# Kernel tuning notes

Measured on AMD Instinct MI355X. Metric: run time of the kernel, lower is better.

## Reference

```python
import jax, jax.numpy as jnp
import numpy as np

B, T, S, D, H, E, K, FF = 4, 1024, 1024, 1024, 16, 8, 2, 4096
DH = D // H
EPS = 1e-5

def layernorm(x, g, b):
    m = x.mean(-1, keepdims=True)
    v = x.var(-1, keepdims=True)
    return (x - m) / jnp.sqrt(v + EPS) * g + b

def mha(q, k, v, mask, wq, bq, wk, bk, wv, bv, wo, bo):
    Bq, Tq, _ = q.shape
    Tk = k.shape[1]
    Q = (q @ wq + bq).reshape(Bq, Tq, H, DH).transpose(0, 2, 1, 3)
    Kh = (k @ wk + bk).reshape(Bq, Tk, H, DH).transpose(0, 2, 1, 3)
    V = (v @ wv + bv).reshape(Bq, Tk, H, DH).transpose(0, 2, 1, 3)
    scores = jnp.einsum('bhqd,bhkd->bhqk', Q, Kh) / (DH ** 0.5)
    scores = jnp.where(mask != 0, scores, jnp.float32(-1e9))
    A = jax.nn.softmax(scores, axis=-1)
    O = jnp.einsum('bhqk,bhkd->bhqd', A, V).transpose(0, 2, 1, 3).reshape(Bq, Tq, D)
    return O @ wo + bo

def sparse_moe(x, wg, bg, w1, b1, w2, b2):
    # x: [B,T,D] -> tokens [N,D]
    Bx, Tx, _ = x.shape
    xt = x.reshape(-1, D)
    N = xt.shape[0]
    probs = jax.nn.softmax(xt @ wg + bg, axis=-1)          # [N,E]
    topv, topi = jax.lax.top_k(probs, K)                    # [N,K]
    topv = topv / topv.sum(-1, keepdims=True)
    gates = jnp.zeros((N, E), xt.dtype).at[jnp.arange(N)[:, None], topi].set(topv)
    h = jax.nn.relu(jnp.einsum('nd,edh->enh', xt, w1) + b1[:, None, :])  # [E,N,FF]
    y = jnp.einsum('enh,ehd->end', h, w2) + b2[:, None, :]               # [E,N,D]
    out = jnp.einsum('ne,end->nd', gates, y)
    return out.reshape(Bx, Tx, D)

def setup_inputs() -> dict:
    key = jax.random.key(0)
    ks = jax.random.split(key, 32)
    r = lambda k, s: jax.random.normal(k, s, dtype=jnp.float32) * 0.02
    inp = {
        'x': jax.random.normal(ks[0], (B, T, D), jnp.float32),
        'encoder_out': jax.random.normal(ks[1], (B, S, D), jnp.float32),
        'src_attn_mask': jnp.ones((B, 1, 1, S), jnp.int32),
        'tgt_attn_mask': jnp.tril(jnp.ones((T, T), jnp.int32))[None, None],
        'ln1_g': jnp.ones((D,), jnp.float32), 'ln1_b': jnp.zeros((D,), jnp.float32),
        'ln2_g': jnp.ones((D,), jnp.float32), 'ln2_b': jnp.zeros((D,), jnp.float32),
        'ln3_g': jnp.ones((D,), jnp.float32), 'ln3_b': jnp.zeros((D,), jnp.float32),
        'wq1': r(ks[2], (D, D)), 'bq1': jnp.zeros((D,), jnp.float32),
        'wk1': r(ks[3], (D, D)), 'bk1': jnp.zeros((D,), jnp.float32),
        'wv1': r(ks[4], (D, D)), 'bv1': jnp.zeros((D,), jnp.float32),
        'wo1': r(ks[5], (D, D)), 'bo1': jnp.zeros((D,), jnp.float32),
        'wq2': r(ks[6], (D, D)), 'bq2': jnp.zeros((D,), jnp.float32),
        'wk2': r(ks[7], (D, D)), 'bk2': jnp.zeros((D,), jnp.float32),
        'wv2': r(ks[8], (D, D)), 'bv2': jnp.zeros((D,), jnp.float32),
        'wo2': r(ks[9], (D, D)), 'bo2': jnp.zeros((D,), jnp.float32),
        'wg': r(ks[10], (D, E)), 'bg': jnp.zeros((E,), jnp.float32),
        'w1': r(ks[11], (E, D, FF)), 'b1': jnp.zeros((E, FF), jnp.float32),
        'w2': r(ks[12], (E, FF, D)), 'b2': jnp.zeros((E, D), jnp.float32),
    }
    return inp

def reference(x, encoder_out, src_attn_mask, tgt_attn_mask,
              ln1_g, ln1_b, ln2_g, ln2_b, ln3_g, ln3_b,
              wq1, bq1, wk1, bk1, wv1, bv1, wo1, bo1,
              wq2, bq2, wk2, bk2, wv2, bv2, wo2, bo2,
              wg, bg, w1, b1, w2, b2):
    # pre-norm residual: x + sublayer(LN(x)); dropout=0 (eval)
    n1 = layernorm(x, ln1_g, ln1_b)
    h1 = x + mha(n1, n1, n1, tgt_attn_mask, wq1, bq1, wk1, bk1, wv1, bv1, wo1, bo1)
    n2 = layernorm(h1, ln2_g, ln2_b)
    h2 = h1 + mha(n2, encoder_out, encoder_out, src_attn_mask, wq2, bq2, wk2, bk2, wv2, bv2, wo2, bo2)
    n3 = layernorm(h2, ln3_g, ln3_b)
    h3 = h2 + sparse_moe(n3, wg, bg, w1, b1, w2, b2)
    return h3
```

## Files before the change

kernel.cpp:

```cpp
#include <hip/hip_runtime.h>

typedef unsigned short u16;
typedef float f32x4 __attribute__((ext_vector_type(4)));
typedef short s16x8 __attribute__((ext_vector_type(8)));
typedef u16   u16x4 __attribute__((ext_vector_type(4)));

#define DEV static __device__ __forceinline__

DEV u16 f2b(float f){
  unsigned u = __builtin_bit_cast(unsigned, f);
  u += 0x7fffu + ((u >> 16) & 1u);
  return (u16)(u >> 16);
}
DEV float b2f(u16 h){ unsigned u = ((unsigned)h) << 16; return __builtin_bit_cast(float, u); }
DEV void tsplit(float v, u16& hv, u16& lv){
  unsigned u = __builtin_bit_cast(unsigned, v);
  hv = (u16)(u >> 16);
  float rest = v - __builtin_bit_cast(float, u & 0xffff0000u);
  lv = (u16)(__builtin_bit_cast(unsigned, rest) >> 16);
}
DEV float fexp2(float x){ float r; asm("v_exp_f32 %0, %1" : "=v"(r) : "v"(x)); return r; }

DEV void glds16(const u16* g, u16* l){
  __builtin_amdgcn_global_load_lds(
      (const __attribute__((address_space(1))) void*)g,
      (__attribute__((address_space(3))) void*)l, 16, 0, 0);
}

DEV f32x4 mfma3(s16x8 ah, s16x8 al, s16x8 bh, s16x8 bl, f32x4 c){
  c = __builtin_amdgcn_mfma_f32_16x16x32_bf16(ah, bh, c, 0, 0, 0);
  c = __builtin_amdgcn_mfma_f32_16x16x32_bf16(ah, bl, c, 0, 0, 0);
  c = __builtin_amdgcn_mfma_f32_16x16x32_bf16(al, bh, c, 0, 0, 0);
  return c;
}

constexpr int TT = 1024, DM = 1024, NE = 8, FFD = 4096;
constexpr int NTOK = 4096;

struct Ptr8 { const float* p[8]; };

__global__ __launch_bounds__(256) void trans8_k(Ptr8 srcs, u16* __restrict__ dh, u16* __restrict__ dl){
  __shared__ float tl[64][65];
  const float* src = srcs.p[blockIdx.z];
  u16* dsth = dh + (size_t)blockIdx.z * 1024 * 1024;
  u16* dstl = dl + (size_t)blockIdx.z * 1024 * 1024;
  const int tid = threadIdx.x;
  const int r0 = blockIdx.y * 64, c0 = blockIdx.x * 64;
  const int ty = tid >> 4, tx = tid & 15;
#pragma unroll
  for (int i = 0; i < 4; i++){
    int row = ty + i * 16;
    f32x4 v = *(const f32x4*)&src[(size_t)(r0 + row) * 1024 + c0 + tx * 4];
#pragma unroll
    for (int j = 0; j < 4; j++) tl[row][tx * 4 + j] = v[j];
  }
  __syncthreads();
#pragma unroll
  for (int i = 0; i < 4; i++){
    int drow = ty + i * 16;
    u16x4 oh, ol;
#pragma unroll
    for (int j = 0; j < 4; j++){
      float v = tl[tx * 4 + j][drow];
      u16 hh, ll; tsplit(v, hh, ll);
      oh[j] = hh; ol[j] = ll;
    }
    *(u16x4*)&dsth[(size_t)(c0 + drow) * 1024 + r0 + tx * 4] = oh;
    *(u16x4*)&dstl[(size_t)(c0 + drow) * 1024 + r0 + tx * 4] = ol;
  }
}

__global__ __launch_bounds__(256) void transb_k(const float* __restrict__ src0, u16* __restrict__ dst0, int R, int C){
  __shared__ float tl[64][65];
  const float* src = src0 + (size_t)blockIdx.z * R * C;
  u16* dst = dst0 + (size_t)blockIdx.z * R * C;
  const int tid = threadIdx.x;
  const int r0 = blockIdx.y * 64, c0 = blockIdx.x * 64;
  const int ty = tid >> 4, tx = tid & 15;
#pragma unroll
  for (int i = 0; i < 4; i++){
    int row = ty + i * 16;
    f32x4 v = *(const f32x4*)&src[(size_t)(r0 + row) * C + c0 + tx * 4];
#pragma unroll
    for (int j = 0; j < 4; j++) tl[row][tx * 4 + j] = v[j];
  }
  __syncthreads();
#pragma unroll
  for (int i = 0; i < 4; i++){
    int drow = ty + i * 16;
    u16x4 o;
#pragma unroll
    for (int j = 0; j < 4; j++) o[j] = f2b(tl[tx * 4 + j][drow]);
    *(u16x4*)&dst[(size_t)(c0 + drow) * R + r0 + tx * 4] = o;
  }
}

__global__ __launch_bounds__(256) void split_k(const float* __restrict__ src,
                                               u16* __restrict__ dh, u16* __restrict__ dl, int n4){
  int i = blockIdx.x * 256 + threadIdx.x;
  if (i < n4){
    f32x4 v = *(const f32x4*)&src[(size_t)i * 4];
    u16x4 oh, ol;
#pragma unroll
    for (int j = 0; j < 4; j++){ u16 hh, ll; tsplit(v[j], hh, ll); oh[j] = hh; ol[j] = ll; }
    *(u16x4*)&dh[(size_t)i * 4] = oh;
    *(u16x4*)&dl[(size_t)i * 4] = ol;
  }
}

__global__ __launch_bounds__(256) void ln_k(const float* __restrict__ x, const float* __restrict__ g,
                                            const float* __restrict__ b,
                                            u16* __restrict__ outH, u16* __restrict__ outL){
  __shared__ float red[8];
  const int row = blockIdx.x, tid = threadIdx.x, l = tid & 63, wave = tid >> 6;
  f32x4 v = *(const f32x4*)&x[(size_t)row * DM + tid * 4];
  float s = v[0] + v[1] + v[2] + v[3];
  float sq = v[0]*v[0] + v[1]*v[1] + v[2]*v[2] + v[3]*v[3];
#pragma unroll
  for (int m = 1; m < 64; m <<= 1){ s += __shfl_xor(s, m); sq += __shfl_xor(sq, m); }
  if (l == 0){ red[wave] = s; red[4 + wave] = sq; }
  __syncthreads();
  float tot = red[0] + red[1] + red[2] + red[3];
  float totq = red[4] + red[5] + red[6] + red[7];
  float mean = tot * (1.0f / DM);
  float var = totq * (1.0f / DM) - mean * mean;
  float rstd = rsqrtf(var + 1e-5f);
  f32x4 gg = *(const f32x4*)&g[tid * 4];
  f32x4 bb = *(const f32x4*)&b[tid * 4];
  u16x4 oh, ol;
#pragma unroll
  for (int j = 0; j < 4; j++){
    float y = (v[j] - mean) * rstd * gg[j] + bb[j];
    u16 hh, ll; tsplit(y, hh, ll); oh[j] = hh; ol[j] = ll;
  }
  *(u16x4*)&outH[(size_t)row * DM + tid * 4] = oh;
  if (outL) *(u16x4*)&outL[(size_t)row * DM + tid * 4] = ol;
}

struct QKVArgs {
  const u16* ah[3]; const u16* al[3]; const float* bias[3];
};

__global__ __launch_bounds__(512) void gemm_qkv3_k(
    QKVArgs args, const u16* __restrict__ Bhp, const u16* __restrict__ Blp,
    u16* __restrict__ QH, u16* __restrict__ QL,
    u16* __restrict__ KH, u16* __restrict__ KL,
    u16* __restrict__ VTH, u16* __restrict__ VTL)
{
  constexpr int K = DM;
  __shared__ alignas(16) u16 LAh[2][128 * 32], LAl[2][128 * 32];
  __shared__ alignas(16) u16 LBh[2][128 * 32], LBl[2][128 * 32];
  const int tid = threadIdx.x, l = tid & 63, wave = tid >> 6;
  const int id = blockIdx.x;
  const int mlo = id & 7, nb = (id >> 3) & 7, mhi = (id >> 6) & 3, seg = id >> 8;
  const int m0 = (mlo + 8 * mhi) * 128, n0 = nb * 128;
  const int r0 = tid >> 2, seg8 = (tid & 3) * 8;
  const u16* gAh = args.ah[seg] + (size_t)(m0 + r0) * K + seg8;
  const u16* gAl = args.al[seg] + (size_t)(m0 + r0) * K + seg8;
  const u16* gBh = Bhp + (size_t)(seg * 1024 + n0 + r0) * K + seg8;
  const u16* gBl = Blp + (size_t)(seg * 1024 + n0 + r0) * K + seg8;
  u16* wAh0 = &LAh[0][wave * 512]; u16* wAh1 = &LAh[1][wave * 512];
  u16* wAl0 = &LAl[0][wave * 512]; u16* wAl1 = &LAl[1][wave * 512];
  u16* wBh0 = &LBh[0][wave * 512]; u16* wBh1 = &LBh[1][wave * 512];
  u16* wBl0 = &LBl[0][wave * 512]; u16* wBl1 = &LBl[1][wave * 512];
  f32x4 acc[4][2];
#pragma unroll
  for (int i = 0; i < 4; i++)
#pragma unroll
    for (int j = 0; j < 2; j++) acc[i][j] = f32x4{0.f, 0.f, 0.f, 0.f};
  const int wm = (wave >> 2) * 64, wn = (wave & 3) * 32;
  for (int kt = 0; kt < K; kt += 64){
    __syncthreads();
    glds16(gAh + kt, wAh0); glds16(gAh + kt + 32, wAh1);
    glds16(gAl + kt, wAl0); glds16(gAl + kt + 32, wAl1);
    glds16(gBh + kt, wBh0); glds16(gBh + kt + 32, wBh1);
    glds16(gBl + kt, wBl0); glds16(gBl + kt + 32, wBl1);
    __syncthreads();
#pragma unroll
    for (int p = 0; p < 2; p++){
      s16x8 afh[4], afl[4], bfh[2], bfl[2];
#pragma unroll
      for (int i = 0; i < 4; i++){
        int ar = (wm + i * 16 + (l & 15)) * 32 + (l >> 4) * 8;
        afh[i] = *(const s16x8*)&LAh[p][ar];
        afl[i] = *(const s16x8*)&LAl[p][ar];
      }
#pragma unroll
      for (int j = 0; j < 2; j++){
        int br = (wn + j * 16 + (l & 15)) * 32 + (l >> 4) * 8;
        bfh[j] = *(const s16x8*)&LBh[p][br];
        bfl[j] = *(const s16x8*)&LBl[p][br];
      }
#pragma unroll
      for (int i = 0; i < 4; i++)
#pragma unroll
        for (int j = 0; j < 2; j++)
          acc[i][j] = mfma3(afh[i], afl[i], bfh[j], bfl[j], acc[i][j]);
    }
  }
  const float* bp = args.bias[seg];
  u16* DH = (seg == 0) ? QH : KH;
  u16* DL = (seg == 0) ? QL : KL;
#pragma unroll
  for (int i = 0; i < 4; i++)
#pragma unroll
    for (int r = 0; r < 4; r++){
      int row = m0 + wm + i * 16 + (l >> 4) * 4 + r;
#pragma unroll
      for (int j = 0; j < 2; j++){
        int col = n0 + wn + j * 16 + (l & 15);
        float v = acc[i][j][r] + bp[col];
        u16 hv, lv; tsplit(v, hv, lv);
        if (seg == 2){
          int bb = row >> 10, tq = row & 1023, hh = col >> 6, dd = col & 63;
          size_t vi = ((size_t)((bb << 4) + hh) * 64 + dd) * 1024 + tq;
          VTH[vi] = hv; VTL[vi] = lv;
        } else {
          size_t idx = (size_t)row * 1024 + col;
          DH[idx] = hv; DL[idx] = lv;
        }
      }
    }
}

__global__ __launch_bounds__(256) void gemm_o64_k(
    const u16* __restrict__ Ahp, const u16* __restrict__ Alp,
    const u16* __restrict__ Bhp, const u16* __restrict__ Blp,
    const float* __restrict__ bias, const float* __restrict__ res,
    float* __restrict__ Cf)
{
  constexpr int K = DM;
  __shared__ alignas(16) u16 LAh[64 * 32], LAl[64 * 32];
  __shared__ alignas(16) u16 LBh[64 * 32], LBl[64 * 32];
  const int tid = threadIdx.x, l = tid & 63, wave = tid >> 6;
  const int m0 = blockIdx.y * 64, n0 = blockIdx.x * 64;
  const int rA = tid >> 2, seg8 = (tid & 3) * 8;
  const u16* gAh = Ahp + (size_t)(m0 + rA) * K + seg8;
  const u16* gAl = Alp + (size_t)(m0 + rA) * K + seg8;
  const u16* gBh = Bhp + (size_t)(n0 + rA) * K + seg8;
  const u16* gBl = Blp + (size_t)(n0 + rA) * K + seg8;
  u16* wAh = &LAh[wave * 512]; u16* wAl = &LAl[wave * 512];
  u16* wBh = &LBh[wave * 512]; u16* wBl = &LBl[wave * 512];
  f32x4 acc[2][2];
#pragma unroll
  for (int i = 0; i < 2; i++)
#pragma unroll
    for (int j = 0; j < 2; j++) acc[i][j] = f32x4{0.f, 0.f, 0.f, 0.f};
  const int wm = (wave >> 1) * 32, wn = (wave & 1) * 32;
  for (int kt = 0; kt < K; kt += 32){
    __syncthreads();
    glds16(gAh + kt, wAh);
    glds16(gAl + kt, wAl);
    glds16(gBh + kt, wBh);
    glds16(gBl + kt, wBl);
    __syncthreads();
    s16x8 afh[2], afl[2], bfh[2], bfl[2];
#pragma unroll
    for (int i = 0; i < 2; i++){
      int ar = (wm + i * 16 + (l & 15)) * 32 + (l >> 4) * 8;
      afh[i] = *(const s16x8*)&LAh[ar];
      afl[i] = *(const s16x8*)&LAl[ar];
    }
#pragma unroll
    for (int j = 0; j < 2; j++){
      int br = (wn + j * 16 + (l & 15)) * 32 + (l >> 4) * 8;
      bfh[j] = *(const s16x8*)&LBh[br];
      bfl[j] = *(const s16x8*)&LBl[br];
    }
#pragma unroll
    for (int i = 0; i < 2; i++)
#pragma unroll
      for (int j = 0; j < 2; j++)
        acc[i][j] = mfma3(afh[i], afl[i], bfh[j], bfl[j], acc[i][j]);
  }
#pragma unroll
  for (int i = 0; i < 2; i++)
#pragma unroll
    for (int r = 0; r < 4; r++){
      int row = m0 + wm + i * 16 + (l >> 4) * 4 + r;
#pragma unroll
      for (int j = 0; j < 2; j++){
        int col = n0 + wn + j * 16 + (l & 15);
        size_t idx = (size_t)row * 1024 + col;
        Cf[idx] = acc[i][j][r] + bias[col] + res[idx];
      }
    }
}

template<bool CAUSAL>
__global__ __launch_bounds__(512) void attn5_k(
    const u16* __restrict__ Qh, const u16* __restrict__ Ql,
    const u16* __restrict__ Kh, const u16* __restrict__ Kl,
    const u16* __restrict__ Vth, const u16* __restrict__ Vtl,
    const int* __restrict__ mask,
    float* __restrict__ OP0, float* __restrict__ OP1,
    float* __restrict__ LS0, float* __restrict__ LS1,
    int Tq, int Tk)
{
  constexpr float CS = 0.125f * 1.4426950408889634f;
  __shared__ alignas(16) u16 KhiL[2048], KloL[2048];
  __shared__ alignas(16) u16 VhiL[2048], VloL[2048];
  __shared__ alignas(16) u16 Plh[8][640], Pll[8][640];
  const int tid = threadIdx.x, l = tid & 63, wave = tid >> 6;
  const int id = blockIdx.x;
  const int bh = ((id >> 3) & 7) * 8 + (id & 7);
  const int b = bh >> 4, h = bh & 15;
  const int qt = (id >> 6) & 7, ks = id >> 9;
  const int q0 = qt * 128;
  float* __restrict__ OP = ks ? OP1 : OP0;
  float* __restrict__ LS = ks ? LS1 : LS0;
  const int ktBeg = ks * 512;
  int lim = CAUSAL ? (q0 + 128) : Tk;
  if (lim > Tk) lim = Tk;
  int ktEnd = (ks + 1) * 512;
  if (ktEnd > lim) ktEnd = lim;

  const int qr = q0 + wave * 16 + (l & 15);
  s16x8 qah[2], qal[2];
#pragma unroll
  for (int kb = 0; kb < 2; kb++){
    size_t base = (size_t)(b * Tq + qr) * DM + h * 64 + kb * 32 + (l >> 4) * 8;
    qah[kb] = *(const s16x8*)(Qh + base);
    qal[kb] = *(const s16x8*)(Ql + base);
  }

  const int sHalf = wave >> 2;
  const int sw = wave & 3;
  const int iS = sw * 64 + l;
  const int keyS = iS >> 3, cKS = iS & 7;
  const u16* gK = (sHalf ? Kl : Kh)
      + (size_t)(b * Tk + ktBeg + keyS) * DM + h * 64 + ((cKS ^ (keyS & 7)) * 8);
  u16* dK = (sHalf ? KloL : KhiL) + sw * 512;
  const int dS = iS >> 2, cVS = iS & 3;
  const size_t vgbase = (size_t)bh * 64 * 1024;
  const u16* gV = (sHalf ? Vtl : Vth)
      + vgbase + (size_t)dS * 1024 + ktBeg + ((cVS ^ ((dS >> 1) & 3)) * 8);
  u16* dV = (sHalf ? VloL : VhiL) + sw * 512;

  float lsum[4] = {0.f, 0.f, 0.f, 0.f};
  f32x4 oacc[4];
#pragma unroll
  for (int nb = 0; nb < 4; nb++) oacc[nb] = f32x4{0.f, 0.f, 0.f, 0.f};
  const int qgr = q0 + wave * 16 + (l >> 4) * 4;

  for (int kt = ktBeg; kt < ktEnd; kt += 32){
    __syncthreads();
    glds16(gK, dK); gK += (size_t)32 * DM;
    glds16(gV, dV); gV += 32;
    __syncthreads();

    f32x4 s[2];
#pragma unroll
    for (int n = 0; n < 2; n++){
      s[n] = f32x4{0.f, 0.f, 0.f, 0.f};
      const int key = n * 16 + (l & 15);
      const int sK = (key & 7);
#pragma unroll
      for (int kb = 0; kb < 2; kb++){
        const int cK = kb * 4 + (l >> 4);
        const int off = key * 64 + ((cK ^ sK) * 8);
        s16x8 kh = *(const s16x8*)&KhiL[off];
        s16x8 klo = *(const s16x8*)&KloL[off];
        s[n] = __builtin_amdgcn_mfma_f32_16x16x32_bf16(qah[kb], kh, s[n], 0, 0, 0);
        s[n] = __builtin_amdgcn_mfma_f32_16x16x32_bf16(qah[kb], klo, s[n], 0, 0, 0);
        s[n] = __builtin_amdgcn_mfma_f32_16x16x32_bf16(qal[kb], kh, s[n], 0, 0, 0);
      }
    }
    int key0 = kt + (l & 15), key1 = key0 + 16;
    int mv0 = 1, mv1 = 1;
    if (!CAUSAL && mask){ mv0 = mask[b * Tk + key0]; mv1 = mask[b * Tk + key1]; }
#pragma unroll
    for (int r = 0; r < 4; r++){
      float p0, p1;
      if (CAUSAL){
        int qg = qgr + r;
        p0 = (key0 <= qg) ? fexp2(s[0][r] * CS) : 0.f;
        p1 = (key1 <= qg) ? fexp2(s[1][r] * CS) : 0.f;
      } else {
        p0 = mv0 ? fexp2(s[0][r] * CS) : 0.f;
        p1 = mv1 ? fexp2(s[1][r] * CS) : 0.f;
      }
      lsum[r] += p0 + p1;
      int po = ((l >> 4) * 4 + r) * 40 + (l & 15);
      u16 h0, l0, h1, l1;
      tsplit(p0, h0, l0); tsplit(p1, h1, l1);
      Plh[wave][po] = h0;      Pll[wave][po] = l0;
      Plh[wave][po + 16] = h1; Pll[wave][po + 16] = l1;
    }
    s16x8 pah = *(const s16x8*)&Plh[wave][(l & 15) * 40 + (l >> 4) * 8];
    s16x8 pal = *(const s16x8*)&Pll[wave][(l & 15) * 40 + (l >> 4) * 8];
#pragma unroll
    for (int nb = 0; nb < 4; nb++){
      const int d = nb * 16 + (l & 15);
      const int off = d * 32 + (((l >> 4) ^ ((d >> 1) & 3)) * 8);
      s16x8 vfh = *(const s16x8*)&VhiL[off];
      s16x8 vfl = *(const s16x8*)&VloL[off];
      oacc[nb] = mfma3(pah, pal, vfh, vfl, oacc[nb]);
    }
  }
#pragma unroll
  for (int r = 0; r < 4; r++){
    float s = lsum[r];
    s += __shfl_xor(s, 1); s += __shfl_xor(s, 2);
    s += __shfl_xor(s, 4); s += __shfl_xor(s, 8);
    int qg = qgr + r;
    if ((l & 15) == 0) LS[(size_t)bh * 1024 + qg] = s;
#pragma unroll
    for (int nb = 0; nb < 4; nb++)
      OP[(size_t)(b * Tq + qg) * DM + h * 64 + nb * 16 + (l & 15)] = oacc[nb][r];
  }
}

__global__ __launch_bounds__(256) void norm_k(
    const float* __restrict__ OP0, const float* __restrict__ OP1,
    const float* __restrict__ LS0, const float* __restrict__ LS1,
    u16* __restrict__ Oh, u16* __restrict__ Ol)
{
  const int t = blockIdx.x, c = threadIdx.x * 4;
  const int b = t >> 10, q = t & 1023, h = c >> 6;
  const size_t li = (size_t)(b * 16 + h) * 1024 + q;
  float inv = 1.0f / (LS0[li] + LS1[li]);
  f32x4 o0 = *(const f32x4*)&OP0[(size_t)t * DM + c];
  f32x4 o1 = *(const f32x4*)&OP1[(size_t)t * DM + c];
  u16x4 oh, ol;
#pragma unroll
  for (int j = 0; j < 4; j++){
    float v = (o0[j] + o1[j]) * inv;
    u16 hh, ll; tsplit(v, hh, ll); oh[j] = hh; ol[j] = ll;
  }
  *(u16x4*)&Oh[(size_t)t * DM + c] = oh;
  *(u16x4*)&Ol[(size_t)t * DM + c] = ol;
}

__global__ __launch_bounds__(256) void moe_gate_k(const float* __restrict__ X,
    const float* __restrict__ g3, const float* __restrict__ b3,
    const float* __restrict__ wg, const float* __restrict__ bg,
    int* __restrict__ cnt, int* __restrict__ perm,
    int* __restrict__ toke, int* __restrict__ tokp, float* __restrict__ tokg)
{
  const int wave = threadIdx.x >> 6, l = threadIdx.x & 63;
  const int t = blockIdx.x * 4 + wave;
  float xv[16];
  float s = 0.f, sq = 0.f;
#pragma unroll
  for (int i = 0; i < 16; i++){
    xv[i] = X[(size_t)t * DM + l + i * 64];
    s += xv[i]; sq += xv[i] * xv[i];
  }
#pragma unroll
  for (int m = 1; m < 64; m <<= 1){ s += __shfl_xor(s, m); sq += __shfl_xor(sq, m); }
  float mean = s * (1.0f / DM);
  float var = sq * (1.0f / DM) - mean * mean;
  float rstd = rsqrtf(var + 1e-5f);
  float acc[8];
#pragma unroll
  for (int e = 0; e < 8; e++) acc[e] = 0.f;
#pragma unroll
  for (int i = 0; i < 16; i++){
    int k = l + i * 64;
    float xn = (xv[i] - mean) * rstd * g3[k] + b3[k];
    f32x4 wa = *(const f32x4*)&wg[k * 8];
    f32x4 wb = *(const f32x4*)&wg[k * 8 + 4];
#pragma unroll
    for (int j = 0; j < 4; j++){ acc[j] += xn * wa[j]; acc[4 + j] += xn * wb[j]; }
  }
#pragma unroll
  for (int e = 0; e < 8; e++)
#pragma unroll
    for (int m = 1; m < 64; m <<= 1) acc[e] += __shfl_xor(acc[e], m);
  if (l == 0){
    float lg[8];
#pragma unroll
    for (int e = 0; e < 8; e++) lg[e] = acc[e] + bg[e];
    float mx = lg[0];
#pragma unroll
    for (int e = 1; e < 8; e++) mx = fmaxf(mx, lg[e]);
    float ex[8]; float sum = 0.f;
#pragma unroll
    for (int e = 0; e < 8; e++){ ex[e] = expf(lg[e] - mx); sum += ex[e]; }
    int i0 = 0;
    for (int e = 1; e < 8; e++) if (ex[e] > ex[i0]) i0 = e;
    int i1 = (i0 == 0) ? 1 : 0;
    for (int e = 0; e < 8; e++) if (e != i0 && ex[e] > ex[i1]) i1 = e;
    float p0 = ex[i0] / sum, p1 = ex[i1] / sum;
    float gs = p0 + p1;
    int pos0 = atomicAdd(&cnt[i0], 1);
    int pos1 = atomicAdd(&cnt[i1], 1);
    perm[i0 * 4096 + pos0] = t;
    perm[i1 * 4096 + pos1] = t;
    toke[2 * t] = i0; toke[2 * t + 1] = i1;
    tokp[2 * t] = pos0; tokp[2 * t + 1] = pos1;
    tokg[2 * t] = p0 / gs; tokg[2 * t + 1] = p1 / gs;
  }
}

__global__ void offsets_k(const int* __restrict__ cnt, int* __restrict__ off){
  if (threadIdx.x == 0){
    int a = 0;
    for (int e = 0; e < 8; e++){ off[e] = a; a += cnt[e]; }
  }
}

__global__ __launch_bounds__(512) void gemm_moe1_k(
    const u16* __restrict__ X, const u16* __restrict__ W1t, const float* __restrict__ b1,
    const int* __restrict__ perm, const int* __restrict__ cnt, const int* __restrict__ off,
    u16* __restrict__ Hb)
{
  const int id = blockIdx.x;
  const int e = id & 7;
  const int rest = id >> 3;
  const int n0 = (rest & 31) * 128;
  const int mt = rest >> 5;
  const int Ce = cnt[e];
  if (mt * 128 >= Ce) return;
  __shared__ alignas(16) u16 Asl[2][128 * 32];
  __shared__ alignas(16) u16 Bsl[2][128 * 32];
  const int tid = threadIdx.x, l = tid & 63, wave = tid >> 6;
  const int r0 = tid >> 2, seg = (tid & 3) * 8;
  const int rl = mt * 128 + r0;
  const int g = perm[e * 4096 + (rl < Ce ? rl : Ce - 1)];
  const u16* gA = X + (size_t)g * DM + seg;
  const u16* gB = W1t + (size_t)e * FFD * DM + (size_t)(n0 + r0) * DM + seg;
  u16* wA0 = &Asl[0][wave * 512]; u16* wA1 = &Asl[1][wave * 512];
  u16* wB0 = &Bsl[0][wave * 512]; u16* wB1 = &Bsl[1][wave * 512];
  f32x4 acc[4][2];
#pragma unroll
  for (int i = 0; i < 4; i++)
#pragma unroll
    for (int j = 0; j < 2; j++) acc[i][j] = f32x4{0.f,0.f,0.f,0.f};
  const int wm = (wave >> 2) * 64, wn = (wave & 3) * 32;
  for (int kt = 0; kt < DM; kt += 64){
    __syncthreads();
    glds16(gA + kt, wA0);
    glds16(gA + kt + 32, wA1);
    glds16(gB + kt, wB0);
    glds16(gB + kt + 32, wB1);
    __syncthreads();
#pragma unroll
    for (int p = 0; p < 2; p++){
      s16x8 af[4], bfr[2];
#pragma unroll
      for (int i = 0; i < 4; i++)
        af[i]  = *(const s16x8*)&Asl[p][(wm + i * 16 + (l & 15)) * 32 + (l >> 4) * 8];
#pragma unroll
      for (int j = 0; j < 2; j++)
        bfr[j] = *(const s16x8*)&Bsl[p][(wn + j * 16 + (l & 15)) * 32 + (l >> 4) * 8];
#pragma unroll
      for (int i = 0; i < 4; i++)
#pragma unroll
        for (int j = 0; j < 2; j++)
          acc[i][j] = __builtin_amdgcn_mfma_f32_16x16x32_bf16(af[i], bfr[j], acc[i][j], 0, 0, 0);
    }
  }
  const int base = off[e];
#pragma unroll
  for (int i = 0; i < 4; i++)
#pragma unroll
    for (int r = 0; r < 4; r++){
      int rloc = mt * 128 + wm + i * 16 + (l >> 4) * 4 + r;
      if (rloc < Ce){
#pragma unroll
        for (int j = 0; j < 2; j++){
          int col = n0 + wn + j * 16 + (l & 15);
          float v = acc[i][j][r] + b1[e * FFD + col];
          v = fmaxf(v, 0.f);
          Hb[(size_t)(base + rloc) * FFD + col] = f2b(v);
        }
      }
    }
}

__global__ __launch_bounds__(512) void gemm_moe2_k(
    const u16* __restrict__ Hb, const u16* __restrict__ W2t,
    const int* __restrict__ cnt, const int* __restrict__ off, float* __restrict__ Y)
{
  const int id = blockIdx.x;
  const int e = id & 7;
  const int rest = id >> 3;
  const int n0 = (rest & 7) * 128;
  const int mt = rest >> 3;
  const int Ce = cnt[e];
  if (mt * 128 >= Ce) return;
  __shared__ alignas(16) u16 Asl[2][128 * 32];
  __shared__ alignas(16) u16 Bsl[2][128 * 32];
  const int tid = threadIdx.x, l = tid & 63, wave = tid >> 6;
  const int r0 = tid >> 2, seg = (tid & 3) * 8;
  const int base = off[e];
  const int rl = mt * 128 + r0;
  const int ar = base + (rl < Ce ? rl : Ce - 1);
  const u16* gA = Hb + (size_t)ar * FFD + seg;
  const u16* gB = W2t + (size_t)e * DM * FFD + (size_t)(n0 + r0) * FFD + seg;
  u16* wA0 = &Asl[0][wave * 512]; u16* wA1 = &Asl[1][wave * 512];
  u16* wB0 = &Bsl[0][wave * 512]; u16* wB1 = &Bsl[1][wave * 512];
  f32x4 acc[4][2];
#pragma unroll
  for (int i = 0; i < 4; i++)
#pragma unroll
    for (int j = 0; j < 2; j++) acc[i][j] = f32x4{0.f,0.f,0.f,0.f};
  const int wm = (wave >> 2) * 64, wn = (wave & 3) * 32;
  for (int kt = 0; kt < FFD; kt += 64){
    __syncthreads();
    glds16(gA + kt, wA0);
    glds16(gA + kt + 32, wA1);
    glds16(gB + kt, wB0);
    glds16(gB + kt + 32, wB1);
    __syncthreads();
#pragma unroll
    for (int p = 0; p < 2; p++){
      s16x8 af[4], bfr[2];
#pragma unroll
      for (int i = 0; i < 4; i++)
        af[i]  = *(const s16x8*)&Asl[p][(wm + i * 16 + (l & 15)) * 32 + (l >> 4) * 8];
#pragma unroll
      for (int j = 0; j < 2; j++)
        bfr[j] = *(const s16x8*)&Bsl[p][(wn + j * 16 + (l & 15)) * 32 + (l >> 4) * 8];
#pragma unroll
      for (int i = 0; i < 4; i++)
#pragma unroll
        for (int j = 0; j < 2; j++)
          acc[i][j] = __builtin_amdgcn_mfma_f32_16x16x32_bf16(af[i], bfr[j], acc[i][j], 0, 0, 0);
    }
  }
#pragma unroll
  for (int i = 0; i < 4; i++)
#pragma unroll
    for (int r = 0; r < 4; r++){
      int rloc = mt * 128 + wm + i * 16 + (l >> 4) * 4 + r;
      if (rloc < Ce){
#pragma unroll
        for (int j = 0; j < 2; j++){
          int col = n0 + wn + j * 16 + (l & 15);
          Y[(size_t)(base + rloc) * DM + col] = acc[i][j][r];
        }
      }
    }
}

__global__ __launch_bounds__(256) void combine_k(const float* __restrict__ h2,
    const float* __restrict__ Y,
    const int* __restrict__ toke, const int* __restrict__ tokp, const float* __restrict__ tokg,
    const int* __restrict__ off, const float* __restrict__ b2, float* __restrict__ out)
{
  const int t = blockIdx.x;
  const int c = threadIdx.x * 4;
  int e0 = toke[2 * t], e1 = toke[2 * t + 1];
  size_t r0 = (size_t)off[e0] + tokp[2 * t];
  size_t r1 = (size_t)off[e1] + tokp[2 * t + 1];
  float g0 = tokg[2 * t], g1 = tokg[2 * t + 1];
  f32x4 a  = *(const f32x4*)&h2[(size_t)t * DM + c];
  f32x4 y0 = *(const f32x4*)&Y[r0 * DM + c];
  f32x4 y1 = *(const f32x4*)&Y[r1 * DM + c];
  f32x4 v0 = *(const f32x4*)&b2[(size_t)e0 * DM + c];
  f32x4 v1 = *(const f32x4*)&b2[(size_t)e1 * DM + c];
  f32x4 o = a + (y0 + v0) * g0 + (y1 + v1) * g1;
  *(f32x4*)&out[(size_t)t * DM + c] = o;
}

extern "C" void kernel_launch(void* const* d_in, const int* in_sizes, int n_in,
                              void* d_out, int out_size, void* d_ws, size_t ws_size,
                              hipStream_t stream) {
  const float* x    = (const float*)d_in[0];
  const float* enc  = (const float*)d_in[1];
  const int* smask  = (const int*)d_in[2];
  const float* ln1g = (const float*)d_in[4]; const float* ln1b = (const float*)d_in[5];
  const float* ln2g = (const float*)d_in[6]; const float* ln2b = (const float*)d_in[7];
  const float* ln3g = (const float*)d_in[8]; const float* ln3b = (const float*)d_in[9];
  const float* wq1 = (const float*)d_in[10]; const float* bq1 = (const float*)d_in[11];
  const float* wk1 = (const float*)d_in[12]; const float* bk1 = (const float*)d_in[13];
  const float* wv1 = (const float*)d_in[14]; const float* bv1 = (const float*)d_in[15];
  const float* wo1 = (const float*)d_in[16]; const float* bo1 = (const float*)d_in[17];
  const float* wq2 = (const float*)d_in[18]; const float* bq2 = (const float*)d_in[19];
  const float* wk2 = (const float*)d_in[20]; const float* bk2 = (const float*)d_in[21];
  const float* wv2 = (const float*)d_in[22]; const float* bv2 = (const float*)d_in[23];
  const float* wo2 = (const float*)d_in[24]; const float* bo2 = (const float*)d_in[25];
  const float* wg  = (const float*)d_in[26]; const float* bg  = (const float*)d_in[27];
  const float* w1  = (const float*)d_in[28]; const float* b1  = (const float*)d_in[29];
  const float* w2  = (const float*)d_in[30]; const float* b2  = (const float*)d_in[31];

  const size_t MB = 1024ull * 1024ull;
  char* ws = (char*)d_ws;
  size_t o = 0;
  auto alloc = [&](size_t bytes) -> void* {
    void* p = ws + o;
    o += (bytes + 255) & ~(size_t)255;
    return p;
  };
  float* H1  = (float*)alloc(16 * MB);
  float* H2  = (float*)alloc(16 * MB);
  u16*  NBF  = (u16*) alloc(8 * MB);
  int* CNT  = (int*)alloc(256);
  int* OFF  = (int*)alloc(256);
  int* PERM = (int*)alloc((size_t)8 * 4096 * 4);
  int* TOKE = (int*)alloc((size_t)NTOK * 2 * 4);
  int* TOKP = (int*)alloc((size_t)NTOK * 2 * 4);
  float* TOKG = (float*)alloc((size_t)NTOK * 2 * 4);
  char* R = (char*)alloc(224 * MB);
  u16* WTH = (u16*)(R);
  u16* WTL = (u16*)(R + 16 * MB);
  u16* NH  = (u16*)(R + 32 * MB);
  u16* NL  = (u16*)(R + 40 * MB);
  u16* EH  = (u16*)(R + 48 * MB);
  u16* EL  = (u16*)(R + 56 * MB);
  u16* QH  = (u16*)(R + 64 * MB);
  u16* QL  = (u16*)(R + 72 * MB);
  u16* KH  = (u16*)(R + 80 * MB);
  u16* KL  = (u16*)(R + 88 * MB);
  u16* VTH = (u16*)(R + 96 * MB);
  u16* VTL = (u16*)(R + 104 * MB);
  u16* OH  = (u16*)(R + 112 * MB);
  u16* OL  = (u16*)(R + 120 * MB);
  float* OP0 = (float*)(R + 128 * MB);
  float* OP1 = (float*)(R + 144 * MB);
  float* LS0 = (float*)(R + 160 * MB);
  float* LS1 = (float*)(R + 161 * MB);
  u16* W1T = (u16*)(R);
  u16* W2T = (u16*)(R + 64 * MB);
  u16* HB  = (u16*)(R + 128 * MB);
  float* YB = (float*)(R + 192 * MB);

  Ptr8 p8; p8.p[0]=wq1; p8.p[1]=wk1; p8.p[2]=wv1; p8.p[3]=wo1;
           p8.p[4]=wq2; p8.p[5]=wk2; p8.p[6]=wv2; p8.p[7]=wo2;
  trans8_k<<<dim3(16,16,8), 256, 0, stream>>>(p8, WTH, WTL);
  split_k<<<dim3(4096), 256, 0, stream>>>(enc, EH, EL, NTOK * DM / 4);

  const size_t W = (size_t)1024 * 1024;
  ln_k<<<dim3(NTOK), 256, 0, stream>>>(x, ln1g, ln1b, NH, NL);
  {
    QKVArgs a;
    a.ah[0]=NH; a.ah[1]=NH; a.ah[2]=NH;
    a.al[0]=NL; a.al[1]=NL; a.al[2]=NL;
    a.bias[0]=bq1; a.bias[1]=bk1; a.bias[2]=bv1;
    gemm_qkv3_k<<<dim3(768), 512, 0, stream>>>(a, WTH + 0*W, WTL + 0*W,
                                               QH, QL, KH, KL, VTH, VTL);
  }
  attn5_k<true><<<dim3(1024), 512, 0, stream>>>(QH, QL, KH, KL, VTH, VTL, nullptr,
                                                OP0, OP1, LS0, LS1, TT, TT);
  norm_k<<<dim3(NTOK), 256, 0, stream>>>(OP0, OP1, LS0, LS1, OH, OL);
  gemm_o64_k<<<dim3(16,64), 256, 0, stream>>>(OH, OL, WTH + 3*W, WTL + 3*W, bo1, x, H1);

  ln_k<<<dim3(NTOK), 256, 0, stream>>>(H1, ln2g, ln2b, NH, NL);
  {
    QKVArgs a;
    a.ah[0]=NH; a.ah[1]=EH; a.ah[2]=EH;
    a.al[0]=NL; a.al[1]=EL; a.al[2]=EL;
    a.bias[0]=bq2; a.bias[1]=bk2; a.bias[2]=bv2;
    gemm_qkv3_k<<<dim3(768), 512, 0, stream>>>(a, WTH + 4*W, WTL + 4*W,
                                               QH, QL, KH, KL, VTH, VTL);
  }
  attn5_k<false><<<dim3(1024), 512, 0, stream>>>(QH, QL, KH, KL, VTH, VTL, smask,
                                                 OP0, OP1, LS0, LS1, TT, TT);
  norm_k<<<dim3(NTOK), 256, 0, stream>>>(OP0, OP1, LS0, LS1, OH, OL);
  gemm_o64_k<<<dim3(16,64), 256, 0, stream>>>(OH, OL, WTH + 7*W, WTL + 7*W, bo2, H1, H2);

  transb_k<<<dim3(64,16,8), 256, 0, stream>>>(w1, W1T, 1024, 4096);
  transb_k<<<dim3(16,64,8), 256, 0, stream>>>(w2, W2T, 4096, 1024);
  ln_k<<<dim3(NTOK), 256, 0, stream>>>(H2, ln3g, ln3b, NBF, nullptr);
  hipMemsetAsync(CNT, 0, 8 * sizeof(int), stream);
  moe_gate_k<<<dim3(1024), 256, 0, stream>>>(H2, ln3g, ln3b, wg, bg, CNT, PERM, TOKE, TOKP, TOKG);
  offsets_k<<<dim3(1), 64, 0, stream>>>(CNT, OFF);
  gemm_moe1_k<<<dim3(8192), 512, 0, stream>>>(NBF, W1T, b1, PERM, CNT, OFF, HB);
  gemm_moe2_k<<<dim3(2048), 512, 0, stream>>>(HB, W2T, CNT, OFF, YB);
  combine_k<<<dim3(NTOK), 256, 0, stream>>>(H2, YB, TOKE, TOKP, TOKG, OFF, b2, (float*)d_out);
}
```

Measured before the change: 807.4 us.

## Double-buffer LDS tiles in MoE expert GEMMs to overlap loads with MFMA

Both MoE GEMM kernels now keep two LDS stages. The global-to-LDS loads for the next K tile are issued before the MFMA work on the current tile, and an explicit vmcnt wait plus barriers replaces the two syncthreads per iteration. This hides global load latency behind compute. In exchange it doubles LDS use per block (64KB), which may reduce occupancy, and it relies on hand-counted vmcnt values being correct.

```diff
diff --git a/kernel.cpp b/kernel.cpp
--- a/kernel.cpp
+++ b/kernel.cpp
@@ -513,44 +513,53 @@
   const int mt = rest >> 5;
   const int Ce = cnt[e];
   if (mt * 128 >= Ce) return;
-  __shared__ alignas(16) u16 Asl[2][128 * 32];
-  __shared__ alignas(16) u16 Bsl[2][128 * 32];
+  __shared__ alignas(16) u16 Asl[2][2][128 * 32];
+  __shared__ alignas(16) u16 Bsl[2][2][128 * 32];
   const int tid = threadIdx.x, l = tid & 63, wave = tid >> 6;
   const int r0 = tid >> 2, seg = (tid & 3) * 8;
   const int rl = mt * 128 + r0;
   const int g = perm[e * 4096 + (rl < Ce ? rl : Ce - 1)];
   const u16* gA = X + (size_t)g * DM + seg;
   const u16* gB = W1t + (size_t)e * FFD * DM + (size_t)(n0 + r0) * DM + seg;
-  u16* wA0 = &Asl[0][wave * 512]; u16* wA1 = &Asl[1][wave * 512];
-  u16* wB0 = &Bsl[0][wave * 512]; u16* wB1 = &Bsl[1][wave * 512];
+  const int wo = wave * 512;
   f32x4 acc[4][2];
 #pragma unroll
   for (int i = 0; i < 4; i++)
 #pragma unroll
     for (int j = 0; j < 2; j++) acc[i][j] = f32x4{0.f,0.f,0.f,0.f};
   const int wm = (wave >> 2) * 64, wn = (wave & 3) * 32;
-  for (int kt = 0; kt < DM; kt += 64){
-    __syncthreads();
-    glds16(gA + kt, wA0);
-    glds16(gA + kt + 32, wA1);
-    glds16(gB + kt, wB0);
-    glds16(gB + kt + 32, wB1);
-    __syncthreads();
+  glds16(gA,      &Asl[0][0][wo]); glds16(gA + 32, &Asl[0][1][wo]);
+  glds16(gB,      &Bsl[0][0][wo]); glds16(gB + 32, &Bsl[0][1][wo]);
+  constexpr int NT = DM / 64;
+  for (int t = 0; t < NT; t++){
+    const int cur = t & 1, nxt = cur ^ 1;
+    if (t < NT - 1){
+      const int kt = (t + 1) * 64;
+      glds16(gA + kt,      &Asl[nxt][0][wo]); glds16(gA + kt + 32, &Asl[nxt][1][wo]);
+      glds16(gB + kt,      &Bsl[nxt][0][wo]); glds16(gB + kt + 32, &Bsl[nxt][1][wo]);
+      asm volatile("s_waitcnt vmcnt(4)" ::: "memory");
+    } else {
+      asm volatile("s_waitcnt vmcnt(0)" ::: "memory");
+    }
+    __builtin_amdgcn_s_barrier();
+    __builtin_amdgcn_sched_barrier(0);
 #pragma unroll
     for (int p = 0; p < 2; p++){
       s16x8 af[4], bfr[2];
 #pragma unroll
       for (int i = 0; i < 4; i++)
-        af[i]  = *(const s16x8*)&Asl[p][(wm + i * 16 + (l & 15)) * 32 + (l >> 4) * 8];
+        af[i]  = *(const s16x8*)&Asl[cur][p][(wm + i * 16 + (l & 15)) * 32 + (l >> 4) * 8];
 #pragma unroll
       for (int j = 0; j < 2; j++)
-        bfr[j] = *(const s16x8*)&Bsl[p][(wn + j * 16 + (l & 15)) * 32 + (l >> 4) * 8];
+        bfr[j] = *(const s16x8*)&Bsl[cur][p][(wn + j * 16 + (l & 15)) * 32 + (l >> 4) * 8];
 #pragma unroll
       for (int i = 0; i < 4; i++)
 #pragma unroll
         for (int j = 0; j < 2; j++)
           acc[i][j] = __builtin_amdgcn_mfma_f32_16x16x32_bf16(af[i], bfr[j], acc[i][j], 0, 0, 0);
     }
+    __builtin_amdgcn_sched_barrier(0);
+    __builtin_amdgcn_s_barrier();
   }
   const int base = off[e];
 #pragma unroll
@@ -581,8 +590,8 @@
   const int mt = rest >> 3;
   const int Ce = cnt[e];
   if (mt * 128 >= Ce) return;
-  __shared__ alignas(16) u16 Asl[2][128 * 32];
-  __shared__ alignas(16) u16 Bsl[2][128 * 32];
+  __shared__ alignas(16) u16 Asl[2][2][128 * 32];
+  __shared__ alignas(16) u16 Bsl[2][2][128 * 32];
   const int tid = threadIdx.x, l = tid & 63, wave = tid >> 6;
   const int r0 = tid >> 2, seg = (tid & 3) * 8;
   const int base = off[e];
@@ -590,36 +599,45 @@
   const int ar = base + (rl < Ce ? rl : Ce - 1);
   const u16* gA = Hb + (size_t)ar * FFD + seg;
   const u16* gB = W2t + (size_t)e * DM * FFD + (size_t)(n0 + r0) * FFD + seg;
-  u16* wA0 = &Asl[0][wave * 512]; u16* wA1 = &Asl[1][wave * 512];
-  u16* wB0 = &Bsl[0][wave * 512]; u16* wB1 = &Bsl[1][wave * 512];
+  const int wo = wave * 512;
   f32x4 acc[4][2];
 #pragma unroll
   for (int i = 0; i < 4; i++)
 #pragma unroll
     for (int j = 0; j < 2; j++) acc[i][j] = f32x4{0.f,0.f,0.f,0.f};
   const int wm = (wave >> 2) * 64, wn = (wave & 3) * 32;
-  for (int kt = 0; kt < FFD; kt += 64){
-    __syncthreads();
-    glds16(gA + kt, wA0);
-    glds16(gA + kt + 32, wA1);
-    glds16(gB + kt, wB0);
-    glds16(gB + kt + 32, wB1);
-    __syncthreads();
+  glds16(gA,      &Asl[0][0][wo]); glds16(gA + 32, &Asl[0][1][wo]);
+  glds16(gB,      &Bsl[0][0][wo]); glds16(gB + 32, &Bsl[0][1][wo]);
+  constexpr int NT = FFD / 64;
+  for (int t = 0; t < NT; t++){
+    const int cur = t & 1, nxt = cur ^ 1;
+    if (t < NT - 1){
+      const int kt = (t + 1) * 64;
+      glds16(gA + kt,      &Asl[nxt][0][wo]); glds16(gA + kt + 32, &Asl[nxt][1][wo]);
+      glds16(gB + kt,      &Bsl[nxt][0][wo]); glds16(gB + kt + 32, &Bsl[nxt][1][wo]);
+      asm volatile("s_waitcnt vmcnt(4)" ::: "memory");
+    } else {
+      asm volatile("s_waitcnt vmcnt(0)" ::: "memory");
+    }
+    __builtin_amdgcn_s_barrier();
+    __builtin_amdgcn_sched_barrier(0);
 #pragma unroll
     for (int p = 0; p < 2; p++){
       s16x8 af[4], bfr[2];
 #pragma unroll
       for (int i = 0; i < 4; i++)
-        af[i]  = *(const s16x8*)&Asl[p][(wm + i * 16 + (l & 15)) * 32 + (l >> 4) * 8];
+        af[i]  = *(const s16x8*)&Asl[cur][p][(wm + i * 16 + (l & 15)) * 32 + (l >> 4) * 8];
 #pragma unroll
       for (int j = 0; j < 2; j++)
-        bfr[j] = *(const s16x8*)&Bsl[p][(wn + j * 16 + (l & 15)) * 32 + (l >> 4) * 8];
+        bfr[j] = *(const s16x8*)&Bsl[cur][p][(wn + j * 16 + (l & 15)) * 32 + (l >> 4) * 8];
 #pragma unroll
       for (int i = 0; i < 4; i++)
 #pragma unroll
         for (int j = 0; j < 2; j++)
           acc[i][j] = __builtin_amdgcn_mfma_f32_16x16x32_bf16(af[i], bfr[j], acc[i][j], 0, 0, 0);
     }
+    __builtin_amdgcn_sched_barrier(0);
+    __builtin_amdgcn_s_barrier();
   }
 #pragma unroll
   for (int i = 0; i < 4; i++)
```

Result: slower. 865.8 us (+7.2%).
